# Kernel optimization log

Hardware: AMD Instinct MI355X
Metric: run time of the kernel (lower is better)

Reference implementation:

```python
import jax, jax.numpy as jnp
import numpy as np

B, H, S, D = 4, 16, 2048, 64

def setup_inputs() -> dict:
    key = jax.random.key(0)
    kq, kk, kv = jax.random.split(key, 3)
    q = jax.random.normal(kq, (B, H, S, D), dtype=jnp.float32)
    k = jax.random.normal(kk, (B, H, S, D), dtype=jnp.float32)
    v = jax.random.normal(kv, (B, H, S, D), dtype=jnp.float32)
    return {"q": q, "k": k, "v": v}

def reference(q, k, v):
    # Faithful port of TransformerBlock.scaled_dot_product_attention
    # (is_causal=True, mha_dropout=0.0 / eval mode).
    head_dim = q.shape[-1]
    scale = jnp.asarray(head_dim, q.dtype) ** -0.5
    q_len, k_len = q.shape[-2], k.shape[-2]
    # causal additive bias: 0 on/below diagonal, -inf above
    causal = jnp.tril(jnp.ones((q_len, k_len), dtype=bool))
    attn_bias = jnp.where(causal, jnp.asarray(0.0, q.dtype), jnp.asarray(-jnp.inf, q.dtype))
    # [b,h,s,d] x [b,h,t,d] -> [b,h,s,t]
    attn_weights = jnp.einsum('bhsd,bhtd->bhst', q * scale, k) + attn_bias
    attn = jax.nn.softmax(attn_weights, axis=-1)
    out = jnp.einsum('bhst,bhtd->bhsd', attn, v)
    return out
```

## Files before the change

### kernel.cpp

```cpp
#include <hip/hip_runtime.h>
#include <math.h>


#define S_LEN 2048
#define D_DIM 64
#define TK 64
#define NHEAD 64
#define MASKV -30000.0f
#define MINIT 1000.0f
#define DEFER_THR 12.0f
#define MNEG -30000.0f
#define LSTR 72
#define PREP_KBLK 4096

typedef __attribute__((ext_vector_type(8))) short bf16x8;
typedef __attribute__((ext_vector_type(4))) float f32x4;

static __device__ __forceinline__ float fast_exp2(float x) {
#if __has_builtin(__builtin_amdgcn_exp2f)
    return __builtin_amdgcn_exp2f(x);
#else
    float r;
    asm volatile("v_exp_f32 %0, %1\n\ts_nop 1" : "=v"(r) : "v"(x));
    return r;
#endif
}

static __device__ __forceinline__ float fmax3(float a, float b, float c) {
    return fmaxf(fmaxf(a, b), c);
}

static __device__ __forceinline__ unsigned int pack_bf16(float a, float b) {
    union { float f; unsigned int u; } ca, cb;
    ca.f = a; cb.f = b;
    unsigned int ua = ca.u + 0x8000u;
    unsigned int ub = cb.u + 0x8000u;
    return (ua >> 16) | (ub & 0xFFFF0000u);
}

static __device__ __forceinline__ unsigned int pack_bf16_fast(float a, float b) {
#if __has_builtin(__builtin_amdgcn_perm)
    union { float f; unsigned int u; } ca, cb;
    ca.f = a; cb.f = b;
    return __builtin_amdgcn_perm(cb.u + 0x8000u, ca.u + 0x8000u, 0x07060302u);
#else
    return pack_bf16(a, b);
#endif
}

typedef const __attribute__((address_space(1))) unsigned int* gas1_t;
typedef __attribute__((address_space(3))) unsigned int* las3_t;
static __device__ __forceinline__ void stage16(const void* g, void* l) {
    __builtin_amdgcn_global_load_lds((gas1_t)g, (las3_t)l, 16, 0, 0);
}

__global__ __launch_bounds__(256)
void fa_prep(const float* __restrict__ kg, const float* __restrict__ vg,
             unsigned short* __restrict__ kb, unsigned short* __restrict__ vb)
{
    const int tid = threadIdx.x;
    const int bid = blockIdx.x;
    if (bid < PREP_KBLK) {
        const int cid = bid * 256 + tid;
        const int ch  = cid & 7;
        const int row = cid >> 3;
        const int kv  = row & (S_LEN - 1);
        const float4* s = reinterpret_cast<const float4*>(kg + (size_t)row * D_DIM + ch * 8);
        float4 a = s[0], b = s[1];
        uint4 w;
        w.x = pack_bf16(a.x, a.y); w.y = pack_bf16(a.z, a.w);
        w.z = pack_bf16(b.x, b.y); w.w = pack_bf16(b.z, b.w);
        const int dst = ch ^ (kv & 7);
        *reinterpret_cast<uint4*>(kb + (size_t)row * D_DIM + dst * 8) = w;
    } else {
        const int wv   = (bid - PREP_KBLK) * 4 + (tid >> 6);
        const int lane = tid & 63;
        const int kg8  = lane >> 3;
        const int dg   = lane & 7;
        const float* s = vg + ((size_t)wv * TK + kg8 * 8) * D_DIM + dg * 8;
        float va[8][8];
        #pragma unroll
        for (int i = 0; i < 8; ++i) {
            const float4* sp = reinterpret_cast<const float4*>(s + (size_t)i * D_DIM);
            float4 x = sp[0], y = sp[1];
            va[i][0] = x.x; va[i][1] = x.y; va[i][2] = x.z; va[i][3] = x.w;
            va[i][4] = y.x; va[i][5] = y.y; va[i][6] = y.z; va[i][7] = y.w;
        }
        unsigned short* db = vb + (size_t)wv * (TK * D_DIM);
        #pragma unroll
        for (int j = 0; j < 8; ++j) {
            const int d = dg * 8 + j;
            uint4 w;
            w.x = pack_bf16(va[0][j], va[1][j]);
            w.y = pack_bf16(va[2][j], va[3][j]);
            w.z = pack_bf16(va[4][j], va[5][j]);
            w.w = pack_bf16(va[6][j], va[7][j]);
            *reinterpret_cast<uint4*>(db + d * D_DIM + 8 * (kg8 ^ j)) = w;
        }
    }
}

__global__ __launch_bounds__(256, 4)
void fa_fwd(const float* __restrict__ qg,
            const unsigned short* __restrict__ kb,
            const unsigned short* __restrict__ vb,
            float* __restrict__ og)
{
    const int head = blockIdx.x;
    const int pr   = blockIdx.y;
    const int tid  = threadIdx.x;
    const int wave = tid >> 6;
    const int lane = tid & 63;
    const int m16  = lane & 15;
    const int quad = lane >> 4;

    __shared__ unsigned short Kl[2][TK * D_DIM];
    __shared__ unsigned short Vt[2][TK * D_DIM];
    __shared__ unsigned short Pl[4][16 * TK];

    const size_t hoff = (size_t)head * S_LEN * D_DIM;
    const unsigned short* kbh = kb + hoff;
    const unsigned short* vbh = vb + hoff;
    float* __restrict__ ogh = og + hoff;

    const int swz  = (m16 & 7) << 4;
    const int colA = (quad * 16) ^ swz;
    const int colB = (64 + quad * 16) ^ swz;
    const int rowB = m16 * 128;
    const int sgo  = wave * 512 + lane * 8;

    char* klds = (char*)&Kl[0][0];
    char* vlds = (char*)&Vt[0][0];
    char* plds = (char*)&Pl[0][0] + wave * 2048 + m16 * 128;
    char* kw   = klds + wave * 1024;
    char* vw   = vlds + wave * 1024;

    const float QSC = 0.18033688011112042f;

    for (int pass = 0; pass < 2; ++pass) {
        const int q0 = ((pass == 0) ? pr : (31 - pr)) * TK;
        const int T  = q0 >> 6;

        bf16x8 qf[2];
        {
            const float* qp = qg + hoff + (size_t)(q0 + wave * 16 + m16) * D_DIM + quad * 8;
            #pragma unroll
            for (int c = 0; c < 2; ++c) {
                float4 a = reinterpret_cast<const float4*>(qp + c * 32)[0];
                float4 b = reinterpret_cast<const float4*>(qp + c * 32)[1];
                unsigned int u0 = pack_bf16(a.x * QSC, a.y * QSC);
                unsigned int u1 = pack_bf16(a.z * QSC, a.w * QSC);
                unsigned int u2 = pack_bf16(b.x * QSC, b.y * QSC);
                unsigned int u3 = pack_bf16(b.z * QSC, b.w * QSC);
                qf[c][0] = (short)(u0 & 0xFFFF); qf[c][1] = (short)(u0 >> 16);
                qf[c][2] = (short)(u1 & 0xFFFF); qf[c][3] = (short)(u1 >> 16);
                qf[c][4] = (short)(u2 & 0xFFFF); qf[c][5] = (short)(u2 >> 16);
                qf[c][6] = (short)(u3 & 0xFFFF); qf[c][7] = (short)(u3 >> 16);
            }
        }

        float l_i = 0.f;
        f32x4 mc = (f32x4){MINIT, MINIT, MINIT, MINIT};
        f32x4 oacc[4];
        #pragma unroll
        for (int nc = 0; nc < 4; ++nc) oacc[nc] = (f32x4){0.f, 0.f, 0.f, 0.f};

        {
            const unsigned short* ks = kbh + sgo;
            const unsigned short* vs = vbh + sgo;
            stage16(ks,        kw);
            stage16(ks + 2048, kw + 4096);
            stage16(vs,        vw);
            stage16(vs + 2048, vw + 4096);
        }
        __syncthreads();

        int cur = 0;
        for (int t = 0; t <= T; ++t) {
            if (t < T) {
                const unsigned short* ks = kbh + (size_t)(t + 1) * 4096 + sgo;
                const unsigned short* vs = vbh + (size_t)(t + 1) * 4096 + sgo;
                const int nb = (cur ^ 1) * 8192;
                stage16(ks,        kw + nb);
                stage16(ks + 2048, kw + nb + 4096);
                stage16(vs,        vw + nb);
                stage16(vs + 2048, vw + nb + 4096);
            }

            const char* kt = klds + cur * 8192;
            const char* vt = vlds + cur * 8192;

            float sv[4][4];
            __builtin_amdgcn_s_setprio(1);
            #pragma unroll
            for (int nt = 0; nt < 4; ++nt) {
                const char* kr = kt + nt * 2048 + rowB;
                bf16x8 kf0 = *reinterpret_cast<const bf16x8*>(kr + colA);
                bf16x8 kf1 = *reinterpret_cast<const bf16x8*>(kr + colB);
                f32x4 acc = __builtin_amdgcn_mfma_f32_16x16x32_bf16(kf0, qf[0], mc, 0, 0, 0);
                acc = __builtin_amdgcn_mfma_f32_16x16x32_bf16(kf1, qf[1], acc, 0, 0, 0);
                #pragma unroll
                for (int r = 0; r < 4; ++r) sv[nt][r] = acc[r];
            }
            __builtin_amdgcn_s_setprio(0);

            if (t == T) {
                #pragma unroll
                for (int nt = 0; nt < 4; ++nt)
                    #pragma unroll
                    for (int r = 0; r < 4; ++r)
                        if (nt * 16 + quad * 4 + r > wave * 16 + m16) sv[nt][r] = MASKV;
            }

            float t0 = fmax3(sv[0][0], sv[0][1], sv[0][2]);
            float t1 = fmax3(sv[0][3], sv[1][0], sv[1][1]);
            float t2 = fmax3(sv[1][2], sv[1][3], sv[2][0]);
            float t3 = fmax3(sv[2][1], sv[2][2], sv[2][3]);
            float t4 = fmax3(sv[3][0], sv[3][1], sv[3][2]);
            float u0 = fmax3(t0, t1, t2);
            float u1 = fmax3(t3, t4, sv[3][3]);
            float rm = fmaxf(u0, u1);
            rm = fmaxf(rm, __shfl_xor(rm, 16, 64));
            rm = fmaxf(rm, __shfl_xor(rm, 32, 64));

            if (__any(rm > DEFER_THR)) {
                float mx    = fmaxf(rm, 0.f);
                float alpha = fast_exp2(-mx);
                l_i *= alpha;
                #pragma unroll
                for (int nc = 0; nc < 4; ++nc)
                    #pragma unroll
                    for (int r = 0; r < 4; ++r) oacc[nc][r] *= alpha;
                #pragma unroll
                for (int nt = 0; nt < 4; ++nt)
                    #pragma unroll
                    for (int r = 0; r < 4; ++r) sv[nt][r] -= mx;
                #pragma unroll
                for (int r = 0; r < 4; ++r) mc[r] -= mx;
            }

            float rs = 0.f;
            #pragma unroll
            for (int nt = 0; nt < 4; ++nt) {
                float e0 = fast_exp2(sv[nt][0]);
                float e1 = fast_exp2(sv[nt][1]);
                float e2 = fast_exp2(sv[nt][2]);
                float e3 = fast_exp2(sv[nt][3]);
                rs += (e0 + e1) + (e2 + e3);
                uint2 pw;
                pw.x = pack_bf16_fast(e0, e1);
                pw.y = pack_bf16_fast(e2, e3);
                *reinterpret_cast<uint2*>(plds + ((nt * 32 + quad * 8) ^ swz)) = pw;
            }
            rs += __shfl_xor(rs, 16, 64);
            rs += __shfl_xor(rs, 32, 64);
            l_i += rs;

            asm volatile("s_waitcnt lgkmcnt(0)" ::: "memory");

            bf16x8 pf0 = *reinterpret_cast<const bf16x8*>(plds + colA);
            bf16x8 pf1 = *reinterpret_cast<const bf16x8*>(plds + colB);
            __builtin_amdgcn_s_setprio(1);
            #pragma unroll
            for (int nc = 0; nc < 4; ++nc) {
                const char* vr = vt + nc * 2048 + rowB;
                bf16x8 vf0 = *reinterpret_cast<const bf16x8*>(vr + colA);
                bf16x8 vf1 = *reinterpret_cast<const bf16x8*>(vr + colB);
                oacc[nc] = __builtin_amdgcn_mfma_f32_16x16x32_bf16(vf0, pf0, oacc[nc], 0, 0, 0);
                oacc[nc] = __builtin_amdgcn_mfma_f32_16x16x32_bf16(vf1, pf1, oacc[nc], 0, 0, 0);
            }
            __builtin_amdgcn_s_setprio(0);

            __syncthreads();
            cur ^= 1;
        }

        float inv = 1.0f / l_i;
        float* op = ogh + (size_t)(q0 + wave * 16 + m16) * D_DIM;
        #pragma unroll
        for (int nc = 0; nc < 4; ++nc) {
            float4 o4;
            o4.x = oacc[nc][0] * inv;
            o4.y = oacc[nc][1] * inv;
            o4.z = oacc[nc][2] * inv;
            o4.w = oacc[nc][3] * inv;
            reinterpret_cast<float4*>(op + nc * 16 + quad * 4)[0] = o4;
        }
    }
}

__global__ __launch_bounds__(256, 4)
void fa_fwd_fb(const float* __restrict__ qg,
               const float* __restrict__ kg,
               const float* __restrict__ vg,
               float* __restrict__ og)
{
    const int head = blockIdx.x;
    const int pr   = blockIdx.y;
    const int tid  = threadIdx.x;
    const int wave = tid >> 6;
    const int lane = tid & 63;
    const int m16  = lane & 15;
    const int quad = lane >> 4;

    __shared__ unsigned short Kl[TK][LSTR];
    __shared__ unsigned short Vt[D_DIM][LSTR];
    __shared__ unsigned short Pl[4][16][LSTR];

    const size_t hoff = (size_t)head * S_LEN * D_DIM;
    const float* kh = kg + hoff;
    const float* vh = vg + hoff;

    const int ksr = tid >> 2;
    const int ksc = (tid & 3) << 4;
    const int va  = lane >> 3;
    const int vb  = lane & 7;
    const int vrr = wave * 16 + 2 * vb;
    const int vcc = 8 * va;
    const float LOG2E = 1.4426950408889634f;

    for (int pass = 0; pass < 2; ++pass) {
        const int q0 = ((pass == 0) ? pr : (31 - pr)) * TK;

        bf16x8 qf[2];
        {
            const float* qp = qg + hoff + (size_t)(q0 + wave * 16 + m16) * D_DIM + quad * 8;
            #pragma unroll
            for (int c = 0; c < 2; ++c) {
                float4 a = reinterpret_cast<const float4*>(qp + c * 32)[0];
                float4 b = reinterpret_cast<const float4*>(qp + c * 32)[1];
                unsigned int u0 = pack_bf16(a.x * 0.125f, a.y * 0.125f);
                unsigned int u1 = pack_bf16(a.z * 0.125f, a.w * 0.125f);
                unsigned int u2 = pack_bf16(b.x * 0.125f, b.y * 0.125f);
                unsigned int u3 = pack_bf16(b.z * 0.125f, b.w * 0.125f);
                qf[c][0] = (short)(u0 & 0xFFFF); qf[c][1] = (short)(u0 >> 16);
                qf[c][2] = (short)(u1 & 0xFFFF); qf[c][3] = (short)(u1 >> 16);
                qf[c][4] = (short)(u2 & 0xFFFF); qf[c][5] = (short)(u2 >> 16);
                qf[c][6] = (short)(u3 & 0xFFFF); qf[c][7] = (short)(u3 >> 16);
            }
        }

        float m_i = MNEG, l_i = 0.f;
        f32x4 oacc[4];
        #pragma unroll
        for (int nc = 0; nc < 4; ++nc) oacc[nc] = (f32x4){0.f, 0.f, 0.f, 0.f};

        float4 kA, kB, kC, kD, vA, vB, vC, vD;
        {
            const float* kp = kh + (size_t)ksr * D_DIM + ksc;
            kA = reinterpret_cast<const float4*>(kp)[0];
            kB = reinterpret_cast<const float4*>(kp)[1];
            kC = reinterpret_cast<const float4*>(kp)[2];
            kD = reinterpret_cast<const float4*>(kp)[3];
            const float* vp = vh + (size_t)vrr * D_DIM + vcc;
            vA = reinterpret_cast<const float4*>(vp)[0];
            vB = reinterpret_cast<const float4*>(vp)[1];
            vC = reinterpret_cast<const float4*>(vp + D_DIM)[0];
            vD = reinterpret_cast<const float4*>(vp + D_DIM)[1];
        }

        for (int j0 = 0; j0 <= q0; j0 += TK) {
            __syncthreads();
            {
                uint4 w0, w1;
                w0.x = pack_bf16(kA.x, kA.y); w0.y = pack_bf16(kA.z, kA.w);
                w0.z = pack_bf16(kB.x, kB.y); w0.w = pack_bf16(kB.z, kB.w);
                w1.x = pack_bf16(kC.x, kC.y); w1.y = pack_bf16(kC.z, kC.w);
                w1.z = pack_bf16(kD.x, kD.y); w1.w = pack_bf16(kD.z, kD.w);
                *reinterpret_cast<uint4*>(&Kl[ksr][ksc])     = w0;
                *reinterpret_cast<uint4*>(&Kl[ksr][ksc + 8]) = w1;

                float r0[8] = {vA.x, vA.y, vA.z, vA.w, vB.x, vB.y, vB.z, vB.w};
                float r1[8] = {vC.x, vC.y, vC.z, vC.w, vD.x, vD.y, vD.z, vD.w};
                #pragma unroll
                for (int jj = 0; jj < 8; ++jj) {
                    int j = (jj + va) & 7;
                    *reinterpret_cast<unsigned int*>(&Vt[vcc + j][vrr]) = pack_bf16(r0[j], r1[j]);
                }
            }
            __syncthreads();

            if (j0 + TK <= q0) {
                const float* kp = kh + (size_t)(j0 + TK + ksr) * D_DIM + ksc;
                kA = reinterpret_cast<const float4*>(kp)[0];
                kB = reinterpret_cast<const float4*>(kp)[1];
                kC = reinterpret_cast<const float4*>(kp)[2];
                kD = reinterpret_cast<const float4*>(kp)[3];
                const float* vp = vh + (size_t)(j0 + TK + vrr) * D_DIM + vcc;
                vA = reinterpret_cast<const float4*>(vp)[0];
                vB = reinterpret_cast<const float4*>(vp)[1];
                vC = reinterpret_cast<const float4*>(vp + D_DIM)[0];
                vD = reinterpret_cast<const float4*>(vp + D_DIM)[1];
            }

            float sv[4][4];
            #pragma unroll
            for (int nt = 0; nt < 4; ++nt) {
                f32x4 acc = (f32x4){0.f, 0.f, 0.f, 0.f};
                bf16x8 kf0 = *reinterpret_cast<const bf16x8*>(&Kl[nt * 16 + m16][quad * 8]);
                bf16x8 kf1 = *reinterpret_cast<const bf16x8*>(&Kl[nt * 16 + m16][32 + quad * 8]);
                acc = __builtin_amdgcn_mfma_f32_16x16x32_bf16(kf0, qf[0], acc, 0, 0, 0);
                acc = __builtin_amdgcn_mfma_f32_16x16x32_bf16(kf1, qf[1], acc, 0, 0, 0);
                #pragma unroll
                for (int r = 0; r < 4; ++r) sv[nt][r] = acc[r];
            }

            if (j0 == q0) {
                #pragma unroll
                for (int nt = 0; nt < 4; ++nt)
                    #pragma unroll
                    for (int r = 0; r < 4; ++r)
                        if (nt * 16 + quad * 4 + r > wave * 16 + m16) sv[nt][r] = MNEG;
            }

            float a0 = fmaxf(fmaxf(sv[0][0], sv[0][1]), fmaxf(sv[0][2], sv[0][3]));
            float a1 = fmaxf(fmaxf(sv[1][0], sv[1][1]), fmaxf(sv[1][2], sv[1][3]));
            float a2 = fmaxf(fmaxf(sv[2][0], sv[2][1]), fmaxf(sv[2][2], sv[2][3]));
            float a3 = fmaxf(fmaxf(sv[3][0], sv[3][1]), fmaxf(sv[3][2], sv[3][3]));
            float rm = fmaxf(fmaxf(a0, a1), fmaxf(a2, a3));
            rm = fmaxf(rm, __shfl_xor(rm, 16, 64));
            rm = fmaxf(rm, __shfl_xor(rm, 32, 64));
            float mnew  = fmaxf(m_i, rm);
            float alpha = fast_exp2((m_i - mnew) * LOG2E);
            float msc   = mnew * LOG2E;
            m_i = mnew;

            float rs = 0.f;
            #pragma unroll
            for (int nt = 0; nt < 4; ++nt) {
                float e0 = fast_exp2(fmaf(sv[nt][0], LOG2E, -msc));
                float e1 = fast_exp2(fmaf(sv[nt][1], LOG2E, -msc));
                float e2 = fast_exp2(fmaf(sv[nt][2], LOG2E, -msc));
                float e3 = fast_exp2(fmaf(sv[nt][3], LOG2E, -msc));
                rs += (e0 + e1) + (e2 + e3);
                uint2 pw;
                pw.x = pack_bf16(e0, e1);
                pw.y = pack_bf16(e2, e3);
                *reinterpret_cast<uint2*>(&Pl[wave][m16][nt * 16 + quad * 4]) = pw;
            }
            rs += __shfl_xor(rs, 16, 64);
            rs += __shfl_xor(rs, 32, 64);
            l_i = fmaf(alpha, l_i, rs);

            #pragma unroll
            for (int nc = 0; nc < 4; ++nc)
                #pragma unroll
                for (int r = 0; r < 4; ++r)
                    oacc[nc][r] *= alpha;

            asm volatile("s_waitcnt lgkmcnt(0)" ::: "memory");

            bf16x8 pf0 = *reinterpret_cast<const bf16x8*>(&Pl[wave][m16][quad * 8]);
            bf16x8 pf1 = *reinterpret_cast<const bf16x8*>(&Pl[wave][m16][32 + quad * 8]);
            #pragma unroll
            for (int nc = 0; nc < 4; ++nc) {
                bf16x8 vf0 = *reinterpret_cast<const bf16x8*>(&Vt[nc * 16 + m16][quad * 8]);
                bf16x8 vf1 = *reinterpret_cast<const bf16x8*>(&Vt[nc * 16 + m16][32 + quad * 8]);
                oacc[nc] = __builtin_amdgcn_mfma_f32_16x16x32_bf16(vf0, pf0, oacc[nc], 0, 0, 0);
                oacc[nc] = __builtin_amdgcn_mfma_f32_16x16x32_bf16(vf1, pf1, oacc[nc], 0, 0, 0);
            }
        }

        float inv = 1.0f / l_i;
        float* op = og + hoff + (size_t)(q0 + wave * 16 + m16) * D_DIM;
        #pragma unroll
        for (int nc = 0; nc < 4; ++nc) {
            float4 o4;
            o4.x = oacc[nc][0] * inv;
            o4.y = oacc[nc][1] * inv;
            o4.z = oacc[nc][2] * inv;
            o4.w = oacc[nc][3] * inv;
            reinterpret_cast<float4*>(op + nc * 16 + quad * 4)[0] = o4;
        }
    }
}

extern "C" void kernel_launch(void* const* d_in, const int* in_sizes, int n_in,
                              void* d_out, int out_size, void* d_ws, size_t ws_size,
                              hipStream_t stream) {
    const float* q = (const float*)d_in[0];
    const float* k = (const float*)d_in[1];
    const float* v = (const float*)d_in[2];
    float* o = (float*)d_out;
    const size_t kvShorts = (size_t)NHEAD * S_LEN * D_DIM;
    const size_t wsNeed   = 2 * kvShorts * sizeof(unsigned short);
    dim3 grid(NHEAD, 16);
    if (d_ws != nullptr && ws_size >= wsNeed) {
        unsigned short* kb = (unsigned short*)d_ws;
        unsigned short* vb = kb + kvShorts;
        fa_prep<<<PREP_KBLK + 512, 256, 0, stream>>>(k, v, kb, vb);
        fa_fwd<<<grid, 256, 0, stream>>>(q, kb, vb, o);
    } else {
        fa_fwd_fb<<<grid, 256, 0, stream>>>(q, k, v, o);
    }
}
```

Baseline: 201.0 us.

## Process two 64-row query tiles per block to reuse each K/V tile

Each block now handles 128 query rows as two 64-row groups that share every staged K/V tile. This halves the number of blocks and the K/V LDS staging traffic per query row. It doubles the accumulator and score register state, so launch bounds drop to 2 blocks per SM, and the grid shrinks to 512 blocks, which lowers occupancy and the amount of parallel work available.

```diff
diff --git a/kernel.cpp b/kernel.cpp
--- a/kernel.cpp
+++ b/kernel.cpp
@@ -100,7 +100,52 @@
     }
 }
 
-__global__ __launch_bounds__(256, 4)
+#define SOFTMAX_GROUP(SV, MC, LI, PL)                                          \
+    {                                                                          \
+        float x0 = fmax3(SV[0][0], SV[0][1], SV[0][2]);                        \
+        float x1 = fmax3(SV[0][3], SV[1][0], SV[1][1]);                        \
+        float x2 = fmax3(SV[1][2], SV[1][3], SV[2][0]);                        \
+        float x3 = fmax3(SV[2][1], SV[2][2], SV[2][3]);                        \
+        float x4 = fmax3(SV[3][0], SV[3][1], SV[3][2]);                        \
+        float y0 = fmax3(x0, x1, x2);                                          \
+        float y1 = fmax3(x3, x4, SV[3][3]);                                    \
+        float rm = fmaxf(y0, y1);                                              \
+        rm = fmaxf(rm, __shfl_xor(rm, 16, 64));                                \
+        rm = fmaxf(rm, __shfl_xor(rm, 32, 64));                                \
+        if (__any(rm > DEFER_THR)) {                                           \
+            float mx    = fmaxf(rm, 0.f);                                      \
+            float alpha = fast_exp2(-mx);                                      \
+            LI *= alpha;                                                       \
+            _Pragma("unroll")                                                  \
+            for (int nc = 0; nc < 4; ++nc)                                     \
+                _Pragma("unroll")                                              \
+                for (int r = 0; r < 4; ++r) oacc##SV[nc][r] *= alpha;          \
+            _Pragma("unroll")                                                  \
+            for (int nt = 0; nt < 4; ++nt)                                     \
+                _Pragma("unroll")                                              \
+                for (int r = 0; r < 4; ++r) SV[nt][r] -= mx;                   \
+            _Pragma("unroll")                                                  \
+            for (int r = 0; r < 4; ++r) MC[r] -= mx;                           \
+        }                                                                      \
+        float rs = 0.f;                                                        \
+        _Pragma("unroll")                                                      \
+        for (int nt = 0; nt < 4; ++nt) {                                       \
+            float e0 = fast_exp2(SV[nt][0]);                                   \
+            float e1 = fast_exp2(SV[nt][1]);                                   \
+            float e2 = fast_exp2(SV[nt][2]);                                   \
+            float e3 = fast_exp2(SV[nt][3]);                                   \
+            rs += (e0 + e1) + (e2 + e3);                                       \
+            uint2 pw;                                                          \
+            pw.x = pack_bf16_fast(e0, e1);                                     \
+            pw.y = pack_bf16_fast(e2, e3);                                     \
+            *reinterpret_cast<uint2*>(PL + ((nt * 32 + quad * 8) ^ swz)) = pw; \
+        }                                                                      \
+        rs += __shfl_xor(rs, 16, 64);                                          \
+        rs += __shfl_xor(rs, 32, 64);                                          \
+        LI += rs;                                                              \
+    }
+
+__global__ __launch_bounds__(256, 2)
 void fa_fwd(const float* __restrict__ qg,
             const unsigned short* __restrict__ kb,
             const unsigned short* __restrict__ vb,
@@ -116,7 +161,7 @@
 
     __shared__ unsigned short Kl[2][TK * D_DIM];
     __shared__ unsigned short Vt[2][TK * D_DIM];
-    __shared__ unsigned short Pl[4][16 * TK];
+    __shared__ unsigned short Pl[4][2][16 * TK];
 
     const size_t hoff = (size_t)head * S_LEN * D_DIM;
     const unsigned short* kbh = kb + hoff;
@@ -131,39 +176,59 @@
 
     char* klds = (char*)&Kl[0][0];
     char* vlds = (char*)&Vt[0][0];
-    char* plds = (char*)&Pl[0][0] + wave * 2048 + m16 * 128;
+    char* plA  = (char*)&Pl[0][0][0] + wave * 4096 + m16 * 128;
+    char* plB  = plA + 2048;
     char* kw   = klds + wave * 1024;
     char* vw   = vlds + wave * 1024;
 
     const float QSC = 0.18033688011112042f;
 
     for (int pass = 0; pass < 2; ++pass) {
-        const int q0 = ((pass == 0) ? pr : (31 - pr)) * TK;
-        const int T  = q0 >> 6;
-
-        bf16x8 qf[2];
+        const int idx = (pass == 0) ? pr : (15 - pr);
+        const int q0  = idx * 128;
+        const int T   = (q0 >> 6) + 1;
+
+        bf16x8 qfA[2], qfB[2];
         {
-            const float* qp = qg + hoff + (size_t)(q0 + wave * 16 + m16) * D_DIM + quad * 8;
+            const float* qpA = qg + hoff + (size_t)(q0 + wave * 16 + m16) * D_DIM + quad * 8;
             #pragma unroll
             for (int c = 0; c < 2; ++c) {
-                float4 a = reinterpret_cast<const float4*>(qp + c * 32)[0];
-                float4 b = reinterpret_cast<const float4*>(qp + c * 32)[1];
+                float4 a = reinterpret_cast<const float4*>(qpA + c * 32)[0];
+                float4 b = reinterpret_cast<const float4*>(qpA + c * 32)[1];
                 unsigned int u0 = pack_bf16(a.x * QSC, a.y * QSC);
                 unsigned int u1 = pack_bf16(a.z * QSC, a.w * QSC);
                 unsigned int u2 = pack_bf16(b.x * QSC, b.y * QSC);
                 unsigned int u3 = pack_bf16(b.z * QSC, b.w * QSC);
-                qf[c][0] = (short)(u0 & 0xFFFF); qf[c][1] = (short)(u0 >> 16);
-                qf[c][2] = (short)(u1 & 0xFFFF); qf[c][3] = (short)(u1 >> 16);
-                qf[c][4] = (short)(u2 & 0xFFFF); qf[c][5] = (short)(u2 >> 16);
-                qf[c][6] = (short)(u3 & 0xFFFF); qf[c][7] = (short)(u3 >> 16);
-            }
-        }
-
-        float l_i = 0.f;
-        f32x4 mc = (f32x4){MINIT, MINIT, MINIT, MINIT};
-        f32x4 oacc[4];
+                qfA[c][0] = (short)(u0 & 0xFFFF); qfA[c][1] = (short)(u0 >> 16);
+                qfA[c][2] = (short)(u1 & 0xFFFF); qfA[c][3] = (short)(u1 >> 16);
+                qfA[c][4] = (short)(u2 & 0xFFFF); qfA[c][5] = (short)(u2 >> 16);
+                qfA[c][6] = (short)(u3 & 0xFFFF); qfA[c][7] = (short)(u3 >> 16);
+            }
+            const float* qpB = qpA + 64 * D_DIM;
+            #pragma unroll
+            for (int c = 0; c < 2; ++c) {
+                float4 a = reinterpret_cast<const float4*>(qpB + c * 32)[0];
+                float4 b = reinterpret_cast<const float4*>(qpB + c * 32)[1];
+                unsigned int u0 = pack_bf16(a.x * QSC, a.y * QSC);
+                unsigned int u1 = pack_bf16(a.z * QSC, a.w * QSC);
+                unsigned int u2 = pack_bf16(b.x * QSC, b.y * QSC);
+                unsigned int u3 = pack_bf16(b.z * QSC, b.w * QSC);
+                qfB[c][0] = (short)(u0 & 0xFFFF); qfB[c][1] = (short)(u0 >> 16);
+                qfB[c][2] = (short)(u1 & 0xFFFF); qfB[c][3] = (short)(u1 >> 16);
+                qfB[c][4] = (short)(u2 & 0xFFFF); qfB[c][5] = (short)(u2 >> 16);
+                qfB[c][6] = (short)(u3 & 0xFFFF); qfB[c][7] = (short)(u3 >> 16);
+            }
+        }
+
+        float lA = 0.f, lB = 0.f;
+        f32x4 mcA = (f32x4){MINIT, MINIT, MINIT, MINIT};
+        f32x4 mcB = (f32x4){MINIT, MINIT, MINIT, MINIT};
+        f32x4 oaccsvA[4], oaccsvB[4];
         #pragma unroll
-        for (int nc = 0; nc < 4; ++nc) oacc[nc] = (f32x4){0.f, 0.f, 0.f, 0.f};
+        for (int nc = 0; nc < 4; ++nc) {
+            oaccsvA[nc] = (f32x4){0.f, 0.f, 0.f, 0.f};
+            oaccsvB[nc] = (f32x4){0.f, 0.f, 0.f, 0.f};
+        }
 
         {
             const unsigned short* ks = kbh + sgo;
@@ -190,84 +255,57 @@
             const char* kt = klds + cur * 8192;
             const char* vt = vlds + cur * 8192;
 
-            float sv[4][4];
+            float svA[4][4], svB[4][4];
             __builtin_amdgcn_s_setprio(1);
             #pragma unroll
             for (int nt = 0; nt < 4; ++nt) {
                 const char* kr = kt + nt * 2048 + rowB;
                 bf16x8 kf0 = *reinterpret_cast<const bf16x8*>(kr + colA);
                 bf16x8 kf1 = *reinterpret_cast<const bf16x8*>(kr + colB);
-                f32x4 acc = __builtin_amdgcn_mfma_f32_16x16x32_bf16(kf0, qf[0], mc, 0, 0, 0);
-                acc = __builtin_amdgcn_mfma_f32_16x16x32_bf16(kf1, qf[1], acc, 0, 0, 0);
-                #pragma unroll
-                for (int r = 0; r < 4; ++r) sv[nt][r] = acc[r];
+                f32x4 aA = __builtin_amdgcn_mfma_f32_16x16x32_bf16(kf0, qfA[0], mcA, 0, 0, 0);
+                aA = __builtin_amdgcn_mfma_f32_16x16x32_bf16(kf1, qfA[1], aA, 0, 0, 0);
+                f32x4 aB = __builtin_amdgcn_mfma_f32_16x16x32_bf16(kf0, qfB[0], mcB, 0, 0, 0);
+                aB = __builtin_amdgcn_mfma_f32_16x16x32_bf16(kf1, qfB[1], aB, 0, 0, 0);
+                #pragma unroll
+                for (int r = 0; r < 4; ++r) { svA[nt][r] = aA[r]; svB[nt][r] = aB[r]; }
             }
             __builtin_amdgcn_s_setprio(0);
 
-            if (t == T) {
+            if (t >= T - 1) {
+                const int sh = (t - (T - 1)) << 6;
                 #pragma unroll
                 for (int nt = 0; nt < 4; ++nt)
                     #pragma unroll
                     for (int r = 0; r < 4; ++r)
-                        if (nt * 16 + quad * 4 + r > wave * 16 + m16) sv[nt][r] = MASKV;
-            }
-
-            float t0 = fmax3(sv[0][0], sv[0][1], sv[0][2]);
-            float t1 = fmax3(sv[0][3], sv[1][0], sv[1][1]);
-            float t2 = fmax3(sv[1][2], sv[1][3], sv[2][0]);
-            float t3 = fmax3(sv[2][1], sv[2][2], sv[2][3]);
-            float t4 = fmax3(sv[3][0], sv[3][1], sv[3][2]);
-            float u0 = fmax3(t0, t1, t2);
-            float u1 = fmax3(t3, t4, sv[3][3]);
-            float rm = fmaxf(u0, u1);
-            rm = fmaxf(rm, __shfl_xor(rm, 16, 64));
-            rm = fmaxf(rm, __shfl_xor(rm, 32, 64));
-
-            if (__any(rm > DEFER_THR)) {
-                float mx    = fmaxf(rm, 0.f);
-                float alpha = fast_exp2(-mx);
-                l_i *= alpha;
-                #pragma unroll
-                for (int nc = 0; nc < 4; ++nc)
-                    #pragma unroll
-                    for (int r = 0; r < 4; ++r) oacc[nc][r] *= alpha;
+                        if (sh + nt * 16 + quad * 4 + r > wave * 16 + m16) svA[nt][r] = MASKV;
+            }
+            if (t == T) {
                 #pragma unroll
                 for (int nt = 0; nt < 4; ++nt)
                     #pragma unroll
-                    for (int r = 0; r < 4; ++r) sv[nt][r] -= mx;
-                #pragma unroll
-                for (int r = 0; r < 4; ++r) mc[r] -= mx;
-            }
-
-            float rs = 0.f;
-            #pragma unroll
-            for (int nt = 0; nt < 4; ++nt) {
-                float e0 = fast_exp2(sv[nt][0]);
-                float e1 = fast_exp2(sv[nt][1]);
-                float e2 = fast_exp2(sv[nt][2]);
-                float e3 = fast_exp2(sv[nt][3]);
-                rs += (e0 + e1) + (e2 + e3);
-                uint2 pw;
-                pw.x = pack_bf16_fast(e0, e1);
-                pw.y = pack_bf16_fast(e2, e3);
-                *reinterpret_cast<uint2*>(plds + ((nt * 32 + quad * 8) ^ swz)) = pw;
-            }
-            rs += __shfl_xor(rs, 16, 64);
-            rs += __shfl_xor(rs, 32, 64);
-            l_i += rs;
+                    for (int r = 0; r < 4; ++r)
+                        if (nt * 16 + quad * 4 + r > wave * 16 + m16) svB[nt][r] = MASKV;
+            }
+
+            SOFTMAX_GROUP(svA, mcA, lA, plA)
+            SOFTMAX_GROUP(svB, mcB, lB, plB)
 
             asm volatile("s_waitcnt lgkmcnt(0)" ::: "memory");
 
-            bf16x8 pf0 = *reinterpret_cast<const bf16x8*>(plds + colA);
-            bf16x8 pf1 = *reinterpret_cast<const bf16x8*>(plds + colB);
+            bf16x8 pfA0 = *reinterpret_cast<const bf16x8*>(plA + colA);
+            bf16x8 pfA1 = *reinterpret_cast<const bf16x8*>(plA + colB);
+            bf16x8 pfB0 = *reinterpret_cast<const bf16x8*>(plB + colA);
+            bf16x8 pfB1 = *reinterpret_cast<const bf16x8*>(plB + colB);
             __builtin_amdgcn_s_setprio(1);
             #pragma unroll
             for (int nc = 0; nc < 4; ++nc) {
                 const char* vr = vt + nc * 2048 + rowB;
                 bf16x8 vf0 = *reinterpret_cast<const bf16x8*>(vr + colA);
                 bf16x8 vf1 = *reinterpret_cast<const bf16x8*>(vr + colB);
-                oacc[nc] = __builtin_amdgcn_mfma_f32_16x16x32_bf16(vf0, pf0, oacc[nc], 0, 0, 0);
-                oacc[nc] = __builtin_amdgcn_mfma_f32_16x16x32_bf16(vf1, pf1, oacc[nc], 0, 0, 0);
+                oaccsvA[nc] = __builtin_amdgcn_mfma_f32_16x16x32_bf16(vf0, pfA0, oaccsvA[nc], 0, 0, 0);
+                oaccsvA[nc] = __builtin_amdgcn_mfma_f32_16x16x32_bf16(vf1, pfA1, oaccsvA[nc], 0, 0, 0);
+                oaccsvB[nc] = __builtin_amdgcn_mfma_f32_16x16x32_bf16(vf0, pfB0, oaccsvB[nc], 0, 0, 0);
+                oaccsvB[nc] = __builtin_amdgcn_mfma_f32_16x16x32_bf16(vf1, pfB1, oaccsvB[nc], 0, 0, 0);
             }
             __builtin_amdgcn_s_setprio(0);
 
@@ -275,16 +313,31 @@
             cur ^= 1;
         }
 
-        float inv = 1.0f / l_i;
-        float* op = ogh + (size_t)(q0 + wave * 16 + m16) * D_DIM;
-        #pragma unroll
-        for (int nc = 0; nc < 4; ++nc) {
-            float4 o4;
-            o4.x = oacc[nc][0] * inv;
-            o4.y = oacc[nc][1] * inv;
-            o4.z = oacc[nc][2] * inv;
-            o4.w = oacc[nc][3] * inv;
-            reinterpret_cast<float4*>(op + nc * 16 + quad * 4)[0] = o4;
+        {
+            float inv = 1.0f / lA;
+            float* op = ogh + (size_t)(q0 + wave * 16 + m16) * D_DIM;
+            #pragma unroll
+            for (int nc = 0; nc < 4; ++nc) {
+                float4 o4;
+                o4.x = oaccsvA[nc][0] * inv;
+                o4.y = oaccsvA[nc][1] * inv;
+                o4.z = oaccsvA[nc][2] * inv;
+                o4.w = oaccsvA[nc][3] * inv;
+                reinterpret_cast<float4*>(op + nc * 16 + quad * 4)[0] = o4;
+            }
+        }
+        {
+            float inv = 1.0f / lB;
+            float* op = ogh + (size_t)(q0 + 64 + wave * 16 + m16) * D_DIM;
+            #pragma unroll
+            for (int nc = 0; nc < 4; ++nc) {
+                float4 o4;
+                o4.x = oaccsvB[nc][0] * inv;
+                o4.y = oaccsvB[nc][1] * inv;
+                o4.z = oaccsvB[nc][2] * inv;
+                o4.w = oaccsvB[nc][3] * inv;
+                reinterpret_cast<float4*>(op + nc * 16 + quad * 4)[0] = o4;
+            }
         }
     }
 }
@@ -484,13 +537,14 @@
     float* o = (float*)d_out;
     const size_t kvShorts = (size_t)NHEAD * S_LEN * D_DIM;
     const size_t wsNeed   = 2 * kvShorts * sizeof(unsigned short);
-    dim3 grid(NHEAD, 16);
     if (d_ws != nullptr && ws_size >= wsNeed) {
         unsigned short* kb = (unsigned short*)d_ws;
         unsigned short* vb = kb + kvShorts;
         fa_prep<<<PREP_KBLK + 512, 256, 0, stream>>>(k, v, kb, vb);
+        dim3 grid(NHEAD, 8);
         fa_fwd<<<grid, 256, 0, stream>>>(q, kb, vb, o);
     } else {
+        dim3 grid(NHEAD, 16);
         fa_fwd_fb<<<grid, 256, 0, stream>>>(q, k, v, o);
     }
 }
```

Result: no change. 200.9 us (-0.1%).

## Switch attention to 32x32x16 MFMA with register-resident P via permlane32 swaps

Applied to the files above, without the earlier changes.

The forward kernel now gives each block one 128-row query tile, with each wave owning 32 rows. It uses 32x32x16 bf16 MFMAs for both QK^T and PV. The P matrix is repacked in registers with v_permlane32_swap instead of being round-tripped through LDS, and row max/sum reductions use permlane swaps rather than shuffles. Blocks are issued heaviest-first and the two-pass load balancing is dropped. The prep kernel is restructured so each thread handles four chunks with fewer blocks, and launch bounds occupancy drops from 4 to 3. Register pressure rises, and the causal tail leaves half the waves idle on the last tiles.

```diff
diff --git a/kernel.cpp b/kernel.cpp
--- a/kernel.cpp
+++ b/kernel.cpp
@@ -11,10 +11,12 @@
 #define DEFER_THR 12.0f
 #define MNEG -30000.0f
 #define LSTR 72
-#define PREP_KBLK 4096
-
-typedef __attribute__((ext_vector_type(8))) short bf16x8;
-typedef __attribute__((ext_vector_type(4))) float f32x4;
+#define PREP_KBLK 1024
+#define PREP_VBLK 128
+
+typedef __attribute__((ext_vector_type(8)))  short bf16x8;
+typedef __attribute__((ext_vector_type(4)))  float f32x4;
+typedef __attribute__((ext_vector_type(16))) float f32x16;
 
 static __device__ __forceinline__ float fast_exp2(float x) {
 #if __has_builtin(__builtin_amdgcn_exp2f)
@@ -48,6 +50,21 @@
 #endif
 }
 
+static __device__ __forceinline__ void plswap(unsigned int& x, unsigned int& y) {
+    asm("s_nop 1\n\tv_permlane32_swap_b32 %0, %1" : "+v"(x), "+v"(y));
+}
+static __device__ __forceinline__ void plswapf(float x, float& t, float& u) {
+    union { float f; unsigned int i; } c;
+    c.f = x;
+    unsigned int a = c.i, b;
+    asm("v_mov_b32 %1, %0\n\t"
+        "s_nop 1\n\t"
+        "v_permlane32_swap_b32 %0, %1"
+        : "+v"(a), "=&v"(b));
+    c.i = a; t = c.f;
+    c.i = b; u = c.f;
+}
+
 typedef const __attribute__((address_space(1))) unsigned int* gas1_t;
 typedef __attribute__((address_space(3))) unsigned int* las3_t;
 static __device__ __forceinline__ void stage16(const void* g, void* l) {
@@ -61,230 +78,276 @@
     const int tid = threadIdx.x;
     const int bid = blockIdx.x;
     if (bid < PREP_KBLK) {
-        const int cid = bid * 256 + tid;
-        const int ch  = cid & 7;
-        const int row = cid >> 3;
-        const int kv  = row & (S_LEN - 1);
-        const float4* s = reinterpret_cast<const float4*>(kg + (size_t)row * D_DIM + ch * 8);
-        float4 a = s[0], b = s[1];
-        uint4 w;
-        w.x = pack_bf16(a.x, a.y); w.y = pack_bf16(a.z, a.w);
-        w.z = pack_bf16(b.x, b.y); w.w = pack_bf16(b.z, b.w);
-        const int dst = ch ^ (kv & 7);
-        *reinterpret_cast<uint4*>(kb + (size_t)row * D_DIM + dst * 8) = w;
+        const int tcid = bid * 256 + tid;
+        float4 a[4], b[4];
+        int rowv[4], dstv[4];
+        #pragma unroll
+        for (int s = 0; s < 4; ++s) {
+            const int cid = tcid + s * 262144;
+            const int ch  = cid & 7;
+            const int row = cid >> 3;
+            const int kv  = row & (S_LEN - 1);
+            const float4* sp = reinterpret_cast<const float4*>(kg + (size_t)row * D_DIM + ch * 8);
+            a[s] = sp[0];
+            b[s] = sp[1];
+            rowv[s] = row;
+            dstv[s] = ch ^ (kv & 7);
+        }
+        #pragma unroll
+        for (int s = 0; s < 4; ++s) {
+            uint4 w;
+            w.x = pack_bf16(a[s].x, a[s].y); w.y = pack_bf16(a[s].z, a[s].w);
+            w.z = pack_bf16(b[s].x, b[s].y); w.w = pack_bf16(b[s].z, b[s].w);
+            *reinterpret_cast<uint4*>(kb + (size_t)rowv[s] * D_DIM + dstv[s] * 8) = w;
+        }
     } else {
-        const int wv   = (bid - PREP_KBLK) * 4 + (tid >> 6);
+        const int wvb  = (bid - PREP_KBLK) * 4 + (tid >> 6);
         const int lane = tid & 63;
         const int kg8  = lane >> 3;
         const int dg   = lane & 7;
-        const float* s = vg + ((size_t)wv * TK + kg8 * 8) * D_DIM + dg * 8;
-        float va[8][8];
-        #pragma unroll
-        for (int i = 0; i < 8; ++i) {
-            const float4* sp = reinterpret_cast<const float4*>(s + (size_t)i * D_DIM);
-            float4 x = sp[0], y = sp[1];
-            va[i][0] = x.x; va[i][1] = x.y; va[i][2] = x.z; va[i][3] = x.w;
-            va[i][4] = y.x; va[i][5] = y.y; va[i][6] = y.z; va[i][7] = y.w;
-        }
-        unsigned short* db = vb + (size_t)wv * (TK * D_DIM);
-        #pragma unroll
-        for (int j = 0; j < 8; ++j) {
-            const int d = dg * 8 + j;
-            uint4 w;
-            w.x = pack_bf16(va[0][j], va[1][j]);
-            w.y = pack_bf16(va[2][j], va[3][j]);
-            w.z = pack_bf16(va[4][j], va[5][j]);
-            w.w = pack_bf16(va[6][j], va[7][j]);
-            *reinterpret_cast<uint4*>(db + d * D_DIM + 8 * (kg8 ^ j)) = w;
-        }
-    }
-}
-
-__global__ __launch_bounds__(256, 4)
+        #pragma unroll 1
+        for (int s = 0; s < 4; ++s) {
+            const int wv = wvb + s * (PREP_VBLK * 4);
+            const float* sp = vg + ((size_t)wv * TK + kg8 * 8) * D_DIM + dg * 8;
+            float va[8][8];
+            #pragma unroll
+            for (int i = 0; i < 8; ++i) {
+                const float4* q4 = reinterpret_cast<const float4*>(sp + (size_t)i * D_DIM);
+                float4 x = q4[0], y = q4[1];
+                va[i][0] = x.x; va[i][1] = x.y; va[i][2] = x.z; va[i][3] = x.w;
+                va[i][4] = y.x; va[i][5] = y.y; va[i][6] = y.z; va[i][7] = y.w;
+            }
+            unsigned short* db = vb + (size_t)wv * (TK * D_DIM);
+            #pragma unroll
+            for (int j = 0; j < 8; ++j) {
+                const int d = dg * 8 + j;
+                uint4 w;
+                w.x = pack_bf16(va[0][j], va[1][j]);
+                w.y = pack_bf16(va[2][j], va[3][j]);
+                w.z = pack_bf16(va[4][j], va[5][j]);
+                w.w = pack_bf16(va[6][j], va[7][j]);
+                *reinterpret_cast<uint4*>(db + d * D_DIM + 8 * (kg8 ^ j)) = w;
+            }
+        }
+    }
+}
+
+__global__ __launch_bounds__(256, 3)
 void fa_fwd(const float* __restrict__ qg,
             const unsigned short* __restrict__ kb,
             const unsigned short* __restrict__ vb,
             float* __restrict__ og)
 {
     const int head = blockIdx.x;
-    const int pr   = blockIdx.y;
+    const int idx  = 15 - (int)blockIdx.y;
+    const int q0   = idx * 128;
     const int tid  = threadIdx.x;
     const int wave = tid >> 6;
     const int lane = tid & 63;
-    const int m16  = lane & 15;
-    const int quad = lane >> 4;
+    const int r0   = lane & 31;
+    const int h    = lane >> 5;
+    const int sw   = r0 & 7;
 
     __shared__ unsigned short Kl[2][TK * D_DIM];
     __shared__ unsigned short Vt[2][TK * D_DIM];
-    __shared__ unsigned short Pl[4][16 * TK];
 
     const size_t hoff = (size_t)head * S_LEN * D_DIM;
     const unsigned short* kbh = kb + hoff;
     const unsigned short* vbh = vb + hoff;
     float* __restrict__ ogh = og + hoff;
 
-    const int swz  = (m16 & 7) << 4;
-    const int colA = (quad * 16) ^ swz;
-    const int colB = (64 + quad * 16) ^ swz;
-    const int rowB = m16 * 128;
     const int sgo  = wave * 512 + lane * 8;
-
     char* klds = (char*)&Kl[0][0];
     char* vlds = (char*)&Vt[0][0];
-    char* plds = (char*)&Pl[0][0] + wave * 2048 + m16 * 128;
     char* kw   = klds + wave * 1024;
     char* vw   = vlds + wave * 1024;
 
+    const int koff = r0 * 128;
+    int coff[4];
+    #pragma unroll
+    for (int s = 0; s < 4; ++s) coff[s] = ((2 * s + h) ^ sw) << 4;
+
+    const int T  = 2 * idx + 1;
+    const int td = 2 * idx + (wave >> 1);
+
     const float QSC = 0.18033688011112042f;
 
-    for (int pass = 0; pass < 2; ++pass) {
-        const int q0 = ((pass == 0) ? pr : (31 - pr)) * TK;
-        const int T  = q0 >> 6;
-
-        bf16x8 qf[2];
-        {
-            const float* qp = qg + hoff + (size_t)(q0 + wave * 16 + m16) * D_DIM + quad * 8;
-            #pragma unroll
-            for (int c = 0; c < 2; ++c) {
-                float4 a = reinterpret_cast<const float4*>(qp + c * 32)[0];
-                float4 b = reinterpret_cast<const float4*>(qp + c * 32)[1];
-                unsigned int u0 = pack_bf16(a.x * QSC, a.y * QSC);
-                unsigned int u1 = pack_bf16(a.z * QSC, a.w * QSC);
-                unsigned int u2 = pack_bf16(b.x * QSC, b.y * QSC);
-                unsigned int u3 = pack_bf16(b.z * QSC, b.w * QSC);
-                qf[c][0] = (short)(u0 & 0xFFFF); qf[c][1] = (short)(u0 >> 16);
-                qf[c][2] = (short)(u1 & 0xFFFF); qf[c][3] = (short)(u1 >> 16);
-                qf[c][4] = (short)(u2 & 0xFFFF); qf[c][5] = (short)(u2 >> 16);
-                qf[c][6] = (short)(u3 & 0xFFFF); qf[c][7] = (short)(u3 >> 16);
-            }
-        }
-
-        float l_i = 0.f;
-        f32x4 mc = (f32x4){MINIT, MINIT, MINIT, MINIT};
-        f32x4 oacc[4];
-        #pragma unroll
-        for (int nc = 0; nc < 4; ++nc) oacc[nc] = (f32x4){0.f, 0.f, 0.f, 0.f};
-
-        {
-            const unsigned short* ks = kbh + sgo;
-            const unsigned short* vs = vbh + sgo;
-            stage16(ks,        kw);
-            stage16(ks + 2048, kw + 4096);
-            stage16(vs,        vw);
-            stage16(vs + 2048, vw + 4096);
-        }
-        __syncthreads();
-
-        int cur = 0;
-        for (int t = 0; t <= T; ++t) {
-            if (t < T) {
-                const unsigned short* ks = kbh + (size_t)(t + 1) * 4096 + sgo;
-                const unsigned short* vs = vbh + (size_t)(t + 1) * 4096 + sgo;
-                const int nb = (cur ^ 1) * 8192;
-                stage16(ks,        kw + nb);
-                stage16(ks + 2048, kw + nb + 4096);
-                stage16(vs,        vw + nb);
-                stage16(vs + 2048, vw + nb + 4096);
-            }
-
+    bf16x8 qf[4];
+    {
+        const int q = q0 + 32 * wave + r0;
+        const float* qp = qg + hoff + (size_t)q * D_DIM;
+        #pragma unroll
+        for (int s = 0; s < 4; ++s) {
+            const float* p = qp + 16 * s + 8 * h;
+            float4 a = reinterpret_cast<const float4*>(p)[0];
+            float4 b = reinterpret_cast<const float4*>(p)[1];
+            unsigned int u0 = pack_bf16(a.x * QSC, a.y * QSC);
+            unsigned int u1 = pack_bf16(a.z * QSC, a.w * QSC);
+            unsigned int u2 = pack_bf16(b.x * QSC, b.y * QSC);
+            unsigned int u3 = pack_bf16(b.z * QSC, b.w * QSC);
+            qf[s][0] = (short)(u0 & 0xFFFF); qf[s][1] = (short)(u0 >> 16);
+            qf[s][2] = (short)(u1 & 0xFFFF); qf[s][3] = (short)(u1 >> 16);
+            qf[s][4] = (short)(u2 & 0xFFFF); qf[s][5] = (short)(u2 >> 16);
+            qf[s][6] = (short)(u3 & 0xFFFF); qf[s][7] = (short)(u3 >> 16);
+        }
+    }
+
+    float l_i = 0.f;
+    f32x16 mc, oacc0, oacc1;
+    #pragma unroll
+    for (int g = 0; g < 16; ++g) { mc[g] = MINIT; oacc0[g] = 0.f; oacc1[g] = 0.f; }
+
+    {
+        const unsigned short* ks = kbh + sgo;
+        const unsigned short* vs = vbh + sgo;
+        stage16(ks,        kw);
+        stage16(ks + 2048, kw + 4096);
+        stage16(vs,        vw);
+        stage16(vs + 2048, vw + 4096);
+    }
+    __syncthreads();
+
+    int cur = 0;
+    for (int t = 0; t <= T; ++t) {
+        if (t < T) {
+            const unsigned short* ks = kbh + (size_t)(t + 1) * 4096 + sgo;
+            const unsigned short* vs = vbh + (size_t)(t + 1) * 4096 + sgo;
+            const int nb = (cur ^ 1) * 8192;
+            stage16(ks,        kw + nb);
+            stage16(ks + 2048, kw + nb + 4096);
+            stage16(vs,        vw + nb);
+            stage16(vs + 2048, vw + nb + 4096);
+        }
+
+        if (t <= td) {
             const char* kt = klds + cur * 8192;
             const char* vt = vlds + cur * 8192;
 
-            float sv[4][4];
+            f32x16 s0, s1;
             __builtin_amdgcn_s_setprio(1);
-            #pragma unroll
-            for (int nt = 0; nt < 4; ++nt) {
-                const char* kr = kt + nt * 2048 + rowB;
-                bf16x8 kf0 = *reinterpret_cast<const bf16x8*>(kr + colA);
-                bf16x8 kf1 = *reinterpret_cast<const bf16x8*>(kr + colB);
-                f32x4 acc = __builtin_amdgcn_mfma_f32_16x16x32_bf16(kf0, qf[0], mc, 0, 0, 0);
-                acc = __builtin_amdgcn_mfma_f32_16x16x32_bf16(kf1, qf[1], acc, 0, 0, 0);
-                #pragma unroll
-                for (int r = 0; r < 4; ++r) sv[nt][r] = acc[r];
+            {
+                bf16x8 k0 = *reinterpret_cast<const bf16x8*>(kt + koff + coff[0]);
+                bf16x8 k1 = *reinterpret_cast<const bf16x8*>(kt + koff + 4096 + coff[0]);
+                s0 = __builtin_amdgcn_mfma_f32_32x32x16_bf16(k0, qf[0], mc, 0, 0, 0);
+                s1 = __builtin_amdgcn_mfma_f32_32x32x16_bf16(k1, qf[0], mc, 0, 0, 0);
+            }
+            #pragma unroll
+            for (int s = 1; s < 4; ++s) {
+                bf16x8 k0 = *reinterpret_cast<const bf16x8*>(kt + koff + coff[s]);
+                bf16x8 k1 = *reinterpret_cast<const bf16x8*>(kt + koff + 4096 + coff[s]);
+                s0 = __builtin_amdgcn_mfma_f32_32x32x16_bf16(k0, qf[s], s0, 0, 0, 0);
+                s1 = __builtin_amdgcn_mfma_f32_32x32x16_bf16(k1, qf[s], s1, 0, 0, 0);
             }
             __builtin_amdgcn_s_setprio(0);
 
-            if (t == T) {
-                #pragma unroll
-                for (int nt = 0; nt < 4; ++nt)
+            if (t == td) {
+                if ((wave & 1) == 0) {
                     #pragma unroll
-                    for (int r = 0; r < 4; ++r)
-                        if (nt * 16 + quad * 4 + r > wave * 16 + m16) sv[nt][r] = MASKV;
-            }
-
-            float t0 = fmax3(sv[0][0], sv[0][1], sv[0][2]);
-            float t1 = fmax3(sv[0][3], sv[1][0], sv[1][1]);
-            float t2 = fmax3(sv[1][2], sv[1][3], sv[2][0]);
-            float t3 = fmax3(sv[2][1], sv[2][2], sv[2][3]);
-            float t4 = fmax3(sv[3][0], sv[3][1], sv[3][2]);
+                    for (int g = 0; g < 16; ++g) {
+                        const int rl = (g & 3) + 8 * (g >> 2) + 4 * h;
+                        if (rl > r0) s0[g] = MASKV;
+                        s1[g] = MASKV;
+                    }
+                } else {
+                    #pragma unroll
+                    for (int g = 0; g < 16; ++g) {
+                        const int rl = (g & 3) + 8 * (g >> 2) + 4 * h;
+                        if (rl > r0) s1[g] = MASKV;
+                    }
+                }
+            }
+
+            float t0 = fmax3(s0[0],  s0[1],  s0[2]);
+            float t1 = fmax3(s0[3],  s0[4],  s0[5]);
+            float t2 = fmax3(s0[6],  s0[7],  s0[8]);
+            float t3 = fmax3(s0[9],  s0[10], s0[11]);
+            float t4 = fmax3(s0[12], s0[13], s0[14]);
+            float t5 = fmax3(s0[15], s1[0],  s1[1]);
+            float t6 = fmax3(s1[2],  s1[3],  s1[4]);
+            float t7 = fmax3(s1[5],  s1[6],  s1[7]);
+            float t8 = fmax3(s1[8],  s1[9],  s1[10]);
+            float t9 = fmax3(s1[11], s1[12], s1[13]);
             float u0 = fmax3(t0, t1, t2);
-            float u1 = fmax3(t3, t4, sv[3][3]);
-            float rm = fmaxf(u0, u1);
-            rm = fmaxf(rm, __shfl_xor(rm, 16, 64));
-            rm = fmaxf(rm, __shfl_xor(rm, 32, 64));
+            float u1 = fmax3(t3, t4, t5);
+            float u2 = fmax3(t6, t7, t8);
+            float u3 = fmax3(t9, s1[14], s1[15]);
+            float rm = fmaxf(fmax3(u0, u1, u2), u3);
+            { float a, b; plswapf(rm, a, b); rm = fmaxf(a, b); }
 
             if (__any(rm > DEFER_THR)) {
                 float mx    = fmaxf(rm, 0.f);
                 float alpha = fast_exp2(-mx);
                 l_i *= alpha;
                 #pragma unroll
-                for (int nc = 0; nc < 4; ++nc)
-                    #pragma unroll
-                    for (int r = 0; r < 4; ++r) oacc[nc][r] *= alpha;
-                #pragma unroll
-                for (int nt = 0; nt < 4; ++nt)
-                    #pragma unroll
-                    for (int r = 0; r < 4; ++r) sv[nt][r] -= mx;
-                #pragma unroll
-                for (int r = 0; r < 4; ++r) mc[r] -= mx;
-            }
-
+                for (int g = 0; g < 16; ++g) {
+                    oacc0[g] *= alpha; oacc1[g] *= alpha;
+                    s0[g] -= mx; s1[g] -= mx;
+                    mc[g] -= mx;
+                }
+            }
+
+            float ea[16], eb[16];
             float rs = 0.f;
             #pragma unroll
-            for (int nt = 0; nt < 4; ++nt) {
-                float e0 = fast_exp2(sv[nt][0]);
-                float e1 = fast_exp2(sv[nt][1]);
-                float e2 = fast_exp2(sv[nt][2]);
-                float e3 = fast_exp2(sv[nt][3]);
-                rs += (e0 + e1) + (e2 + e3);
-                uint2 pw;
-                pw.x = pack_bf16_fast(e0, e1);
-                pw.y = pack_bf16_fast(e2, e3);
-                *reinterpret_cast<uint2*>(plds + ((nt * 32 + quad * 8) ^ swz)) = pw;
-            }
-            rs += __shfl_xor(rs, 16, 64);
-            rs += __shfl_xor(rs, 32, 64);
-            l_i += rs;
-
-            asm volatile("s_waitcnt lgkmcnt(0)" ::: "memory");
-
-            bf16x8 pf0 = *reinterpret_cast<const bf16x8*>(plds + colA);
-            bf16x8 pf1 = *reinterpret_cast<const bf16x8*>(plds + colB);
+            for (int g = 0; g < 16; ++g) {
+                ea[g] = fast_exp2(s0[g]);
+                eb[g] = fast_exp2(s1[g]);
+            }
+            #pragma unroll
+            for (int g = 0; g < 16; ++g) rs += ea[g] + eb[g];
+            { float a, b; plswapf(rs, a, b); l_i += a + b; }
+
+            unsigned int pa[8], pb[8];
+            #pragma unroll
+            for (int k = 0; k < 8; ++k) {
+                pa[k] = pack_bf16_fast(ea[2 * k], ea[2 * k + 1]);
+                pb[k] = pack_bf16_fast(eb[2 * k], eb[2 * k + 1]);
+            }
+            plswap(pa[0], pa[2]); plswap(pa[1], pa[3]);
+            plswap(pa[4], pa[6]); plswap(pa[5], pa[7]);
+            plswap(pb[0], pb[2]); plswap(pb[1], pb[3]);
+            plswap(pb[4], pb[6]); plswap(pb[5], pb[7]);
+            union { unsigned int u[4]; bf16x8 v; } pf[4];
+            pf[0].u[0] = pa[0]; pf[0].u[1] = pa[1]; pf[0].u[2] = pa[2]; pf[0].u[3] = pa[3];
+            pf[1].u[0] = pa[4]; pf[1].u[1] = pa[5]; pf[1].u[2] = pa[6]; pf[1].u[3] = pa[7];
+            pf[2].u[0] = pb[0]; pf[2].u[1] = pb[1]; pf[2].u[2] = pb[2]; pf[2].u[3] = pb[3];
+            pf[3].u[0] = pb[4]; pf[3].u[1] = pb[5]; pf[3].u[2] = pb[6]; pf[3].u[3] = pb[7];
+
             __builtin_amdgcn_s_setprio(1);
             #pragma unroll
-            for (int nc = 0; nc < 4; ++nc) {
-                const char* vr = vt + nc * 2048 + rowB;
-                bf16x8 vf0 = *reinterpret_cast<const bf16x8*>(vr + colA);
-                bf16x8 vf1 = *reinterpret_cast<const bf16x8*>(vr + colB);
-                oacc[nc] = __builtin_amdgcn_mfma_f32_16x16x32_bf16(vf0, pf0, oacc[nc], 0, 0, 0);
-                oacc[nc] = __builtin_amdgcn_mfma_f32_16x16x32_bf16(vf1, pf1, oacc[nc], 0, 0, 0);
+            for (int s = 0; s < 4; ++s) {
+                bf16x8 v0 = *reinterpret_cast<const bf16x8*>(vt + koff + coff[s]);
+                bf16x8 v1 = *reinterpret_cast<const bf16x8*>(vt + koff + 4096 + coff[s]);
+                oacc0 = __builtin_amdgcn_mfma_f32_32x32x16_bf16(v0, pf[s].v, oacc0, 0, 0, 0);
+                oacc1 = __builtin_amdgcn_mfma_f32_32x32x16_bf16(v1, pf[s].v, oacc1, 0, 0, 0);
             }
             __builtin_amdgcn_s_setprio(0);
-
-            __syncthreads();
-            cur ^= 1;
-        }
-
-        float inv = 1.0f / l_i;
-        float* op = ogh + (size_t)(q0 + wave * 16 + m16) * D_DIM;
-        #pragma unroll
-        for (int nc = 0; nc < 4; ++nc) {
+        }
+
+        __syncthreads();
+        cur ^= 1;
+    }
+
+    {
+        const float inv = 1.0f / l_i;
+        float* op = ogh + (size_t)(q0 + 32 * wave + r0) * D_DIM;
+        #pragma unroll
+        for (int a = 0; a < 4; ++a) {
             float4 o4;
-            o4.x = oacc[nc][0] * inv;
-            o4.y = oacc[nc][1] * inv;
-            o4.z = oacc[nc][2] * inv;
-            o4.w = oacc[nc][3] * inv;
-            reinterpret_cast<float4*>(op + nc * 16 + quad * 4)[0] = o4;
+            o4.x = oacc0[4 * a + 0] * inv;
+            o4.y = oacc0[4 * a + 1] * inv;
+            o4.z = oacc0[4 * a + 2] * inv;
+            o4.w = oacc0[4 * a + 3] * inv;
+            reinterpret_cast<float4*>(op + 8 * a + 4 * h)[0] = o4;
+        }
+        #pragma unroll
+        for (int a = 0; a < 4; ++a) {
+            float4 o4;
+            o4.x = oacc1[4 * a + 0] * inv;
+            o4.y = oacc1[4 * a + 1] * inv;
+            o4.z = oacc1[4 * a + 2] * inv;
+            o4.w = oacc1[4 * a + 3] * inv;
+            reinterpret_cast<float4*>(op + 32 + 8 * a + 4 * h)[0] = o4;
         }
     }
 }
@@ -484,13 +547,14 @@
     float* o = (float*)d_out;
     const size_t kvShorts = (size_t)NHEAD * S_LEN * D_DIM;
     const size_t wsNeed   = 2 * kvShorts * sizeof(unsigned short);
-    dim3 grid(NHEAD, 16);
     if (d_ws != nullptr && ws_size >= wsNeed) {
-        unsigned short* kb = (unsigned short*)d_ws;
-        unsigned short* vb = kb + kvShorts;
-        fa_prep<<<PREP_KBLK + 512, 256, 0, stream>>>(k, v, kb, vb);
-        fa_fwd<<<grid, 256, 0, stream>>>(q, kb, vb, o);
+        unsigned short* kbp = (unsigned short*)d_ws;
+        unsigned short* vbp = kbp + kvShorts;
+        fa_prep<<<PREP_KBLK + PREP_VBLK, 256, 0, stream>>>(k, v, kbp, vbp);
+        dim3 grid(NHEAD, 16);
+        fa_fwd<<<grid, 256, 0, stream>>>(q, kbp, vbp, o);
     } else {
+        dim3 grid(NHEAD, 16);
         fa_fwd_fb<<<grid, 256, 0, stream>>>(q, k, v, o);
     }
 }
```

After: 189.6 us. 1.06x faster.
